# Performance work log

Measured on AMD Instinct MI355X. Metric: run time of the kernel, lower is better.

The kernel has to match this reference:

```python
import jax, jax.numpy as jnp
import numpy as np

K = 3  # kernel_size
S = 1  # stride
P = 1  # padding


def setup_inputs() -> dict:
    key = jax.random.key(0)
    ks = jax.random.split(key, 5)
    B, C, H, W, O = 4, 64, 128, 128, 64
    x = jax.random.normal(ks[0], (B, C, H, W), jnp.float32)
    # offset conv params (module inits these to 0; use small random values so the
    # bilinear-gather path is actually exercised with non-integer offsets)
    w_off = jax.random.normal(ks[1], (2 * K * K, C, K, K), jnp.float32) * 0.01
    b_off = jax.random.normal(ks[2], (2 * K * K,), jnp.float32) * 0.01
    # deformable conv params (torchvision DeformConv2d has bias=True by default)
    w_dcn = jax.random.normal(ks[3], (O, C, K, K), jnp.float32) * (1.0 / np.sqrt(C * K * K))
    b_dcn = jax.random.normal(ks[4], (O,), jnp.float32) * 0.01
    return {"x": x, "w_off": w_off, "b_off": b_off, "w_dcn": w_dcn, "b_dcn": b_dcn}


def _conv(x, w, b):
    y = jax.lax.conv_general_dilated(
        x, w, window_strides=(S, S), padding=[(P, P), (P, P)],
        dimension_numbers=("NCHW", "OIHW", "NCHW"))
    return y + b[None, :, None, None]


def _deform_conv2d(x, offset, w_dcn, b_dcn):
    # x: [B,C,H,W]; offset: [B, 2*K*K, Ho, Wo] with (dy, dx) interleaved per
    # kernel tap (row-major kh*K+kw), matching torchvision deform_conv2d.
    B, C, H, W = x.shape
    Ho, Wo = offset.shape[2], offset.shape[3]
    K2 = K * K
    off = offset.reshape(B, K2, 2, Ho, Wo)
    oy, ox = off[:, :, 0], off[:, :, 1]  # [B,K2,Ho,Wo]

    kh = (jnp.arange(K2) // K).astype(jnp.float32)
    kw = (jnp.arange(K2) % K).astype(jnp.float32)
    base_y = (jnp.arange(Ho) * S - P).astype(jnp.float32)
    base_x = (jnp.arange(Wo) * S - P).astype(jnp.float32)
    # fractional sampling locations: p0 + p_k + offset
    py = base_y[None, None, :, None] + kh[None, :, None, None] + oy  # [B,K2,Ho,Wo]
    px = base_x[None, None, None, :] + kw[None, :, None, None] + ox

    y0f = jnp.floor(py); x0f = jnp.floor(px)
    dy = py - y0f; dx = px - x0f
    y0 = y0f.astype(jnp.int32); x0 = x0f.astype(jnp.int32)

    def gather(yi, xi):
        # implicit zero padding: mask out-of-range corners
        valid = (yi >= 0) & (yi < H) & (xi >= 0) & (xi < W)
        yc = jnp.clip(yi, 0, H - 1)
        xc = jnp.clip(xi, 0, W - 1)
        v = jax.vmap(lambda xb, yb, xib: xb[:, yb, xib])(x, yc, xc)  # [B,C,K2,Ho,Wo]
        return v * valid[:, None].astype(x.dtype)

    v00 = gather(y0, x0)
    v01 = gather(y0, x0 + 1)
    v10 = gather(y0 + 1, x0)
    v11 = gather(y0 + 1, x0 + 1)

    wy = dy[:, None]; wx = dx[:, None]  # [B,1,K2,Ho,Wo]
    sampled = (v00 * (1 - wy) * (1 - wx) + v01 * (1 - wy) * wx
               + v10 * wy * (1 - wx) + v11 * wy * wx)  # [B,C,K2,Ho,Wo]

    O = w_dcn.shape[0]
    out = jnp.einsum("bckij,ock->boij", sampled, w_dcn.reshape(O, C, K2))
    return out + b_dcn[None, :, None, None]


def reference(x, w_off, b_off, w_dcn, b_dcn):
    offset = _conv(x, w_off, b_off)          # [B, 2*K*K, Ho, Wo]
    return _deform_conv2d(x, offset, w_dcn, b_dcn)
```

## Files before the change

kernel.cpp:

```cpp
#include <hip/hip_runtime.h>
#include <hip/hip_fp16.h>

#define B_ 4
#define H_ 128
#define W_ 128
#define HW_ 16384

typedef _Float16 half8 __attribute__((ext_vector_type(8)));
typedef float floatx16 __attribute__((ext_vector_type(16)));
typedef __attribute__((address_space(3))) void lds_void;
typedef const __attribute__((address_space(1))) void gbl_void;


__global__ __launch_bounds__(256) void k_prep(
    const float* __restrict__ x, const float* __restrict__ w_dcn,
    const float* __restrict__ w_off,
    __half* __restrict__ W2L, __half* __restrict__ W0L,
    _Float16* __restrict__ xh)
{
    int bid = blockIdx.x;
    int t = threadIdx.x;
    if (bid < 2048) {
        int idx = bid*256 + t;
        int p  = idx & (HW_-1);
        int bc = idx >> 14;
        const float* s = x + (size_t)bc*8*HW_ + p;
        half8 vv;
        #pragma unroll
        for (int e = 0; e < 8; ++e) vv[e] = (_Float16)s[e*HW_];
        *(half8*)(xh + (size_t)idx*8) = vv;
    } else {
        int idx = (bid - 2048)*256 + t;
        if (idx < 36864) {
            int e = idx & 7, lane = (idx>>3) & 63, og = (idx>>9) & 1;
            int ks = (idx>>10) & 3, tap = idx >> 12;
            int o = og*32 + (lane & 31);
            int c = ks*16 + (lane >> 5)*8 + e;
            W2L[idx] = __float2half(w_dcn[o*576 + c*9 + tap]);
        } else {
            int i2 = idx - 36864;
            int e = i2 & 7, lane = (i2>>3) & 63;
            int ks = (i2>>9) & 3, tap = i2 >> 11;
            int oc = lane & 31;
            int c = ks*16 + (lane >> 5)*8 + e;
            W0L[i2] = (oc < 18) ? __float2half(w_off[oc*576 + c*9 + tap])
                                : __float2half(0.f);
        }
    }
}

#define CHS2 3456
#define WLOC_OFF 27648
#define SMEM_SZ 36864

__global__ __launch_bounds__(128, 2) void k_fused(
    const float* __restrict__ x, const _Float16* __restrict__ xh,
    const _Float16* __restrict__ W2L, const _Float16* __restrict__ W0L,
    const float* __restrict__ b_off, const float* __restrict__ b_dcn,
    float* __restrict__ out)
{
    __shared__ __attribute__((aligned(16))) char smem[SMEM_SZ];
    char* halo_c = smem;

    int t = threadIdx.x;
    int lane = t & 63;
    int v = __builtin_amdgcn_readfirstlane(t >> 6);
    int c31 = lane & 31;
    int h8  = lane >> 5;

    char*  wl   = smem + WLOC_OFF + v*4608;
    float* offL = (float*)wl;
    char*  desc = wl;

    int bid  = blockIdx.x;
    int xcd  = bid & 7, sidx = bid >> 3;
    int orig = xcd*128 + sidx;
    int b    = orig >> 8;
    int rem  = orig & 255;
    int i0   = (rem >> 2) * 2;
    int j0   = (rem & 3) * 32;

    const float* xf = x + (size_t)b * (64*HW_);

    {
        int nst  = 14 - v;
        int base = v * 14;
        const _Float16* xhb = xh + ((size_t)b << 20);
        for (int s = 0; s < nst; ++s) {
            int i   = base + s;
            int idx = (i << 6) + lane;
            int ch  = idx / 216;
            int pl  = idx - ch*216;
            int hr  = pl / 36;
            int hx  = pl - hr*36;
            int grow = min(max(i0 - 2 + hr, 0), H_-1);
            int gcol = min(max(j0 - 2 + hx, 0), W_-1);
            const _Float16* g = xhb + ((size_t)ch << 17) + (size_t)(((grow<<7) + gcol) << 3);
            __builtin_amdgcn_global_load_lds((gbl_void*)g,
                                             (lds_void*)(halo_c + (i << 10)),
                                             16, 0, 0);
        }
    }
    __syncthreads();

    floatx16 accA = {0.f,0.f,0.f,0.f,0.f,0.f,0.f,0.f,0.f,0.f,0.f,0.f,0.f,0.f,0.f,0.f};
    const half8 hz = {0,0,0,0,0,0,0,0};
    #pragma unroll
    for (int tap = 0; tap < 9; ++tap) {
        int kh = tap/3, kw = tap - (tap/3)*3;
        int ii = i0 + v - 1 + kh;
        int jj = j0 + c31 - 1 + kw;
        bool valid = (ii >= 0) && (ii < H_) && (jj >= 0) && (jj < W_);
        int pixA = (v + 1 + kh)*36 + (c31 + 1 + kw);
        #pragma unroll
        for (int s = 0; s < 4; ++s) {
            half8 a = *(const half8*)(halo_c + (s*2 + h8)*CHS2 + pixA*16);
            a = valid ? a : hz;
            half8 bf = *(const half8*)(W0L + ((tap*4+s)<<9) + (lane<<3));
            accA = __builtin_amdgcn_mfma_f32_32x32x16_f16(a, bf, accA, 0, 0, 0);
        }
    }
    {
        int oc = c31;
        if (oc < 18) {
            float bo = b_off[oc];
            #pragma unroll
            for (int r = 0; r < 16; ++r) {
                int row = (r & 3) + 8*(r >> 2) + 4*h8;
                offL[row*18 + oc] = accA[r] + bo;
            }
        }
    }

    float2 o2r[5];
    #pragma unroll
    for (int e = 0; e < 5; ++e) {
        int idx = e*64 + lane;
        if (idx < 288) {
            int pl = idx / 9, tap = idx - pl*9;
            o2r[e] = *(const float2*)(offL + pl*18 + 2*tap);
        }
    }
    uint4 dreg[5];
    #pragma unroll
    for (int e = 0; e < 5; ++e) {
        int idx = e*64 + lane;
        if (idx < 288) {
            int pl = idx / 9, tap = idx - pl*9;
            int kh = tap/3, kw = tap - (tap/3)*3;
            float py = (float)(i0 + v - 1 + kh) + o2r[e].x;
            float px = (float)(j0 + pl - 1 + kw) + o2r[e].y;
            float y0f = floorf(py), x0f = floorf(px);
            float dy = py - y0f, dx = px - x0f;
            int y0 = (int)y0f, x0i = (int)x0f;
            int y1 = y0 + 1,  x1 = x0i + 1;
            bool vy0 = (y0>=0)&(y0<H_),   vy1 = (y1>=0)&(y1<H_);
            bool vx0 = (x0i>=0)&(x0i<W_), vx1 = (x1>=0)&(x1<W_);
            int yc0 = min(max(y0,0),H_-1),  yc1 = min(max(y1,0),H_-1);
            int xc0 = min(max(x0i,0),W_-1), xc1 = min(max(x1,0),W_-1);
            float w00 = (1.f-dy)*(1.f-dx) * ((vy0&&vx0)?1.f:0.f);
            float w01 = (1.f-dy)*dx       * ((vy0&&vx1)?1.f:0.f);
            float w10 = dy*(1.f-dx)       * ((vy1&&vx0)?1.f:0.f);
            float w11 = dy*dx             * ((vy1&&vx1)?1.f:0.f);
            int hy0 = yc0 - (i0-2), hy1 = yc1 - (i0-2);
            int hx0 = xc0 - (j0-2), hx1 = xc1 - (j0-2);
            bool inh = ((unsigned)hy0 < 6u) & ((unsigned)hy1 < 6u)
                     & ((unsigned)hx0 < 36u) & ((unsigned)hx1 < 36u);
            unsigned a0,a1,a2,a3;
            if (inh) { a0 = hy0*36+hx0; a1 = hy0*36+hx1; a2 = hy1*36+hx0; a3 = hy1*36+hx1; }
            else     { a0 = ((yc0<<7)+xc0) | 0x8000u; a1 = (yc0<<7)+xc1;
                       a2 = (yc1<<7)+xc0;             a3 = (yc1<<7)+xc1; }
            __half2 hw0 = __floats2half2_rn(w00, w01);
            __half2 hw1 = __floats2half2_rn(w10, w11);
            dreg[e].x = a0 | (a1 << 16);
            dreg[e].y = a2 | (a3 << 16);
            dreg[e].z = *(unsigned*)&hw0;
            dreg[e].w = *(unsigned*)&hw1;
        }
    }
    #pragma unroll
    for (int e = 0; e < 5; ++e) {
        int idx = e*64 + lane;
        if (idx < 288) {
            int pl = idx / 9, tap = idx - pl*9;
            *(uint4*)(desc + (tap*32 + pl)*16) = dreg[e];
        }
    }

    floatx16 acc0 = {0.f,0.f,0.f,0.f,0.f,0.f,0.f,0.f,0.f,0.f,0.f,0.f,0.f,0.f,0.f,0.f};
    floatx16 acc1 = acc0;

    const char* hqs0 = halo_c + (0*2 + h8)*CHS2;
    const char* hqs1 = halo_c + (1*2 + h8)*CHS2;
    const char* hqs2 = halo_c + (2*2 + h8)*CHS2;
    const char* hqs3 = halo_c + (3*2 + h8)*CHS2;

    #pragma unroll 3
    for (int tap = 0; tap < 9; ++tap) {
        uint4 d = *(const uint4*)(desc + (tap*32 + c31)*16);
        unsigned p0i = d.x & 0x7fffu, p1i = d.x >> 16;
        unsigned p2i = d.y & 0xffffu, p3i = d.y >> 16;
        bool inh = (d.x & 0x8000u) == 0u;
        unsigned short b00 = (unsigned short)(d.z & 0xffffu);
        unsigned short b01 = (unsigned short)(d.z >> 16);
        unsigned short b10 = (unsigned short)(d.w & 0xffffu);
        unsigned short b11 = (unsigned short)(d.w >> 16);
        _Float16 h00 = *(_Float16*)&b00, h01 = *(_Float16*)&b01;
        _Float16 h10 = *(_Float16*)&b10, h11 = *(_Float16*)&b11;
        half8 W00 = {h00,h00,h00,h00,h00,h00,h00,h00};
        half8 W01 = {h01,h01,h01,h01,h01,h01,h01,h01};
        half8 W10 = {h10,h10,h10,h10,h10,h10,h10,h10};
        half8 W11 = {h11,h11,h11,h11,h11,h11,h11,h11};
        half8 sk[4];
        const char* hb[4] = {hqs0, hqs1, hqs2, hqs3};
        #pragma unroll
        for (int s = 0; s < 4; ++s) {
            half8 v00, v01, v10, v11;
            if (inh) {
                v00 = *(const half8*)(hb[s] + p0i*16);
                v01 = *(const half8*)(hb[s] + p1i*16);
                v10 = *(const half8*)(hb[s] + p2i*16);
                v11 = *(const half8*)(hb[s] + p3i*16);
            } else {
                int chb = (s*2 + h8)*8;
                #pragma unroll
                for (int e = 0; e < 8; ++e) {
                    v00[e] = (_Float16)xf[(chb+e)*HW_ + (int)p0i];
                    v01[e] = (_Float16)xf[(chb+e)*HW_ + (int)p1i];
                    v10[e] = (_Float16)xf[(chb+e)*HW_ + (int)p2i];
                    v11[e] = (_Float16)xf[(chb+e)*HW_ + (int)p3i];
                }
            }
            sk[s] = v00*W00 + v01*W01 + v10*W10 + v11*W11;
        }
        #pragma unroll
        for (int s = 0; s < 4; ++s) {
            half8 bf0 = *(const half8*)(W2L + (((tap*4+s)*2+0)<<9) + (lane<<3));
            acc0 = __builtin_amdgcn_mfma_f32_32x32x16_f16(sk[s], bf0, acc0, 0, 0, 0);
            half8 bf1 = *(const half8*)(W2L + (((tap*4+s)*2+1)<<9) + (lane<<3));
            acc1 = __builtin_amdgcn_mfma_f32_32x32x16_f16(sk[s], bf1, acc1, 0, 0, 0);
        }
    }
    __syncthreads();

    float* E = (float*)smem;
    #pragma unroll
    for (int r = 0; r < 16; ++r) {
        int row = (r & 3) + 8*(r >> 2) + 4*h8;
        int pl  = v*32 + row;
        E[pl*66 + c31]      = acc0[r];
        E[pl*66 + 32 + c31] = acc1[r];
    }
    __syncthreads();
    int obase = (b*64)*HW_ + i0*W_ + j0;
    int prow = (lane >> 5)*W_ + c31;
    #pragma unroll
    for (int rep = 0; rep < 32; ++rep) {
        int o = rep*2 + v;
        out[obase + o*HW_ + prow] = E[lane*66 + o] + b_dcn[o];
    }
}

extern "C" void kernel_launch(void* const* d_in, const int* in_sizes, int n_in,
                              void* d_out, int out_size, void* d_ws, size_t ws_size,
                              hipStream_t stream) {
    const float* x     = (const float*)d_in[0];
    const float* w_off = (const float*)d_in[1];
    const float* b_off = (const float*)d_in[2];
    const float* w_dcn = (const float*)d_in[3];
    const float* b_dcn = (const float*)d_in[4];
    float* out = (float*)d_out;

    __half* W2L = (__half*)d_ws;
    __half* W0L = (__half*)((char*)d_ws + 73728);
    _Float16* xh = (_Float16*)((char*)d_ws + 110592);

    k_prep<<<2264, 256, 0, stream>>>(x, w_dcn, w_off, W2L, W0L, xh);
    k_fused<<<1024, 128, 0, stream>>>(x, xh, (const _Float16*)W2L,
                                      (const _Float16*)W0L, b_off, b_dcn, out);
}
```

Baseline: 92.04 us.

## Split channel reduction across four waves per block with LDS partial-sum combine

Doubles the block to 256 threads so each output row is handled by two waves that each reduce over half of the input channels, then combines the partial accumulators through shared memory. Only half the waves compute the offset conv and sampling descriptors, and the others wait at an added barrier. The out-of-halo fallback now reads packed fp16 channel-vector data instead of eight scalar fp32 loads. The aim is more waves in flight per CU to hide LDS and gather latency, at the cost of extra barriers, idle waves during the offset phase and an LDS reduction step.

```diff
diff --git a/kernel.cpp b/kernel.cpp
--- a/kernel.cpp
+++ b/kernel.cpp
@@ -53,7 +53,7 @@
 #define WLOC_OFF 27648
 #define SMEM_SZ 36864
 
-__global__ __launch_bounds__(128, 2) void k_fused(
+__global__ __launch_bounds__(256, 3) void k_fused(
     const float* __restrict__ x, const _Float16* __restrict__ xh,
     const _Float16* __restrict__ W2L, const _Float16* __restrict__ W0L,
     const float* __restrict__ b_off, const float* __restrict__ b_dcn,
@@ -64,11 +64,13 @@
 
     int t = threadIdx.x;
     int lane = t & 63;
-    int v = __builtin_amdgcn_readfirstlane(t >> 6);
+    int w = __builtin_amdgcn_readfirstlane(t >> 6);
+    int row   = w & 1;
+    int khalf = w >> 1;
     int c31 = lane & 31;
     int h8  = lane >> 5;
 
-    char*  wl   = smem + WLOC_OFF + v*4608;
+    char*  wl   = smem + WLOC_OFF + row*4608;
     float* offL = (float*)wl;
     char*  desc = wl;
 
@@ -80,14 +82,9 @@
     int i0   = (rem >> 2) * 2;
     int j0   = (rem & 3) * 32;
 
-    const float* xf = x + (size_t)b * (64*HW_);
-
     {
-        int nst  = 14 - v;
-        int base = v * 14;
         const _Float16* xhb = xh + ((size_t)b << 20);
-        for (int s = 0; s < nst; ++s) {
-            int i   = base + s;
+        for (int i = w; i < 27; i += 4) {
             int idx = (i << 6) + lane;
             int ch  = idx / 216;
             int pl  = idx - ch*216;
@@ -103,97 +100,100 @@
     }
     __syncthreads();
 
-    floatx16 accA = {0.f,0.f,0.f,0.f,0.f,0.f,0.f,0.f,0.f,0.f,0.f,0.f,0.f,0.f,0.f,0.f};
-    const half8 hz = {0,0,0,0,0,0,0,0};
-    #pragma unroll
-    for (int tap = 0; tap < 9; ++tap) {
-        int kh = tap/3, kw = tap - (tap/3)*3;
-        int ii = i0 + v - 1 + kh;
-        int jj = j0 + c31 - 1 + kw;
-        bool valid = (ii >= 0) && (ii < H_) && (jj >= 0) && (jj < W_);
-        int pixA = (v + 1 + kh)*36 + (c31 + 1 + kw);
-        #pragma unroll
-        for (int s = 0; s < 4; ++s) {
-            half8 a = *(const half8*)(halo_c + (s*2 + h8)*CHS2 + pixA*16);
-            a = valid ? a : hz;
-            half8 bf = *(const half8*)(W0L + ((tap*4+s)<<9) + (lane<<3));
-            accA = __builtin_amdgcn_mfma_f32_32x32x16_f16(a, bf, accA, 0, 0, 0);
-        }
-    }
-    {
-        int oc = c31;
-        if (oc < 18) {
-            float bo = b_off[oc];
+    if (khalf == 0) {
+        floatx16 accA = {0.f,0.f,0.f,0.f,0.f,0.f,0.f,0.f,0.f,0.f,0.f,0.f,0.f,0.f,0.f,0.f};
+        const half8 hz = {0,0,0,0,0,0,0,0};
+        #pragma unroll 3
+        for (int tap = 0; tap < 9; ++tap) {
+            int kh = tap/3, kw = tap - (tap/3)*3;
+            int ii = i0 + row - 1 + kh;
+            int jj = j0 + c31 - 1 + kw;
+            bool valid = (ii >= 0) && (ii < H_) && (jj >= 0) && (jj < W_);
+            int pixA = (row + 1 + kh)*36 + (c31 + 1 + kw);
             #pragma unroll
-            for (int r = 0; r < 16; ++r) {
-                int row = (r & 3) + 8*(r >> 2) + 4*h8;
-                offL[row*18 + oc] = accA[r] + bo;
-            }
-        }
-    }
-
-    float2 o2r[5];
-    #pragma unroll
-    for (int e = 0; e < 5; ++e) {
-        int idx = e*64 + lane;
-        if (idx < 288) {
-            int pl = idx / 9, tap = idx - pl*9;
-            o2r[e] = *(const float2*)(offL + pl*18 + 2*tap);
-        }
-    }
-    uint4 dreg[5];
-    #pragma unroll
-    for (int e = 0; e < 5; ++e) {
-        int idx = e*64 + lane;
-        if (idx < 288) {
-            int pl = idx / 9, tap = idx - pl*9;
-            int kh = tap/3, kw = tap - (tap/3)*3;
-            float py = (float)(i0 + v - 1 + kh) + o2r[e].x;
-            float px = (float)(j0 + pl - 1 + kw) + o2r[e].y;
-            float y0f = floorf(py), x0f = floorf(px);
-            float dy = py - y0f, dx = px - x0f;
-            int y0 = (int)y0f, x0i = (int)x0f;
-            int y1 = y0 + 1,  x1 = x0i + 1;
-            bool vy0 = (y0>=0)&(y0<H_),   vy1 = (y1>=0)&(y1<H_);
-            bool vx0 = (x0i>=0)&(x0i<W_), vx1 = (x1>=0)&(x1<W_);
-            int yc0 = min(max(y0,0),H_-1),  yc1 = min(max(y1,0),H_-1);
-            int xc0 = min(max(x0i,0),W_-1), xc1 = min(max(x1,0),W_-1);
-            float w00 = (1.f-dy)*(1.f-dx) * ((vy0&&vx0)?1.f:0.f);
-            float w01 = (1.f-dy)*dx       * ((vy0&&vx1)?1.f:0.f);
-            float w10 = dy*(1.f-dx)       * ((vy1&&vx0)?1.f:0.f);
-            float w11 = dy*dx             * ((vy1&&vx1)?1.f:0.f);
-            int hy0 = yc0 - (i0-2), hy1 = yc1 - (i0-2);
-            int hx0 = xc0 - (j0-2), hx1 = xc1 - (j0-2);
-            bool inh = ((unsigned)hy0 < 6u) & ((unsigned)hy1 < 6u)
-                     & ((unsigned)hx0 < 36u) & ((unsigned)hx1 < 36u);
-            unsigned a0,a1,a2,a3;
-            if (inh) { a0 = hy0*36+hx0; a1 = hy0*36+hx1; a2 = hy1*36+hx0; a3 = hy1*36+hx1; }
-            else     { a0 = ((yc0<<7)+xc0) | 0x8000u; a1 = (yc0<<7)+xc1;
-                       a2 = (yc1<<7)+xc0;             a3 = (yc1<<7)+xc1; }
-            __half2 hw0 = __floats2half2_rn(w00, w01);
-            __half2 hw1 = __floats2half2_rn(w10, w11);
-            dreg[e].x = a0 | (a1 << 16);
-            dreg[e].y = a2 | (a3 << 16);
-            dreg[e].z = *(unsigned*)&hw0;
-            dreg[e].w = *(unsigned*)&hw1;
-        }
-    }
-    #pragma unroll
-    for (int e = 0; e < 5; ++e) {
-        int idx = e*64 + lane;
-        if (idx < 288) {
-            int pl = idx / 9, tap = idx - pl*9;
-            *(uint4*)(desc + (tap*32 + pl)*16) = dreg[e];
-        }
-    }
+            for (int s = 0; s < 4; ++s) {
+                half8 a = *(const half8*)(halo_c + (s*2 + h8)*CHS2 + pixA*16);
+                a = valid ? a : hz;
+                half8 bf = *(const half8*)(W0L + ((tap*4+s)<<9) + (lane<<3));
+                accA = __builtin_amdgcn_mfma_f32_32x32x16_f16(a, bf, accA, 0, 0, 0);
+            }
+        }
+        {
+            int oc = c31;
+            if (oc < 18) {
+                float bo = b_off[oc];
+                #pragma unroll
+                for (int r = 0; r < 16; ++r) {
+                    int rr = (r & 3) + 8*(r >> 2) + 4*h8;
+                    offL[rr*18 + oc] = accA[r] + bo;
+                }
+            }
+        }
+        float2 o2r[5];
+        #pragma unroll
+        for (int e = 0; e < 5; ++e) {
+            int idx = e*64 + lane;
+            if (idx < 288) {
+                int pl = idx / 9, tap = idx - pl*9;
+                o2r[e] = *(const float2*)(offL + pl*18 + 2*tap);
+            }
+        }
+        uint4 dreg[5];
+        #pragma unroll
+        for (int e = 0; e < 5; ++e) {
+            int idx = e*64 + lane;
+            if (idx < 288) {
+                int pl = idx / 9, tap = idx - pl*9;
+                int kh = tap/3, kw = tap - (tap/3)*3;
+                float py = (float)(i0 + row - 1 + kh) + o2r[e].x;
+                float px = (float)(j0 + pl - 1 + kw) + o2r[e].y;
+                float y0f = floorf(py), x0f = floorf(px);
+                float dy = py - y0f, dx = px - x0f;
+                int y0 = (int)y0f, x0i = (int)x0f;
+                int y1 = y0 + 1,  x1 = x0i + 1;
+                bool vy0 = (y0>=0)&(y0<H_),   vy1 = (y1>=0)&(y1<H_);
+                bool vx0 = (x0i>=0)&(x0i<W_), vx1 = (x1>=0)&(x1<W_);
+                int yc0 = min(max(y0,0),H_-1),  yc1 = min(max(y1,0),H_-1);
+                int xc0 = min(max(x0i,0),W_-1), xc1 = min(max(x1,0),W_-1);
+                float w00 = (1.f-dy)*(1.f-dx) * ((vy0&&vx0)?1.f:0.f);
+                float w01 = (1.f-dy)*dx       * ((vy0&&vx1)?1.f:0.f);
+                float w10 = dy*(1.f-dx)       * ((vy1&&vx0)?1.f:0.f);
+                float w11 = dy*dx             * ((vy1&&vx1)?1.f:0.f);
+                int hy0 = yc0 - (i0-2), hy1 = yc1 - (i0-2);
+                int hx0 = xc0 - (j0-2), hx1 = xc1 - (j0-2);
+                bool inh = ((unsigned)hy0 < 6u) & ((unsigned)hy1 < 6u)
+                         & ((unsigned)hx0 < 36u) & ((unsigned)hx1 < 36u);
+                unsigned a0,a1,a2,a3;
+                if (inh) { a0 = hy0*36+hx0; a1 = hy0*36+hx1; a2 = hy1*36+hx0; a3 = hy1*36+hx1; }
+                else     { a0 = ((yc0<<7)+xc0) | 0x8000u; a1 = (yc0<<7)+xc1;
+                           a2 = (yc1<<7)+xc0;             a3 = (yc1<<7)+xc1; }
+                __half2 hw0 = __floats2half2_rn(w00, w01);
+                __half2 hw1 = __floats2half2_rn(w10, w11);
+                dreg[e].x = a0 | (a1 << 16);
+                dreg[e].y = a2 | (a3 << 16);
+                dreg[e].z = *(unsigned*)&hw0;
+                dreg[e].w = *(unsigned*)&hw1;
+            }
+        }
+        #pragma unroll
+        for (int e = 0; e < 5; ++e) {
+            int idx = e*64 + lane;
+            if (idx < 288) {
+                int pl = idx / 9, tap = idx - pl*9;
+                *(uint4*)(desc + (tap*32 + pl)*16) = dreg[e];
+            }
+        }
+    }
+    __syncthreads();
 
     floatx16 acc0 = {0.f,0.f,0.f,0.f,0.f,0.f,0.f,0.f,0.f,0.f,0.f,0.f,0.f,0.f,0.f,0.f};
     floatx16 acc1 = acc0;
 
-    const char* hqs0 = halo_c + (0*2 + h8)*CHS2;
-    const char* hqs1 = halo_c + (1*2 + h8)*CHS2;
-    const char* hqs2 = halo_c + (2*2 + h8)*CHS2;
-    const char* hqs3 = halo_c + (3*2 + h8)*CHS2;
+    int sA = khalf*2, sB = sA + 1;
+    const char* hq0 = halo_c + (sA*2 + h8)*CHS2;
+    const char* hq1 = halo_c + (sB*2 + h8)*CHS2;
+    const _Float16* xqA = xh + (((size_t)(b*8) + sA*2 + h8) << 17);
+    const _Float16* xqB = xh + (((size_t)(b*8) + sB*2 + h8) << 17);
 
     #pragma unroll 3
     for (int tap = 0; tap < 9; ++tap) {
@@ -211,52 +211,66 @@
         half8 W01 = {h01,h01,h01,h01,h01,h01,h01,h01};
         half8 W10 = {h10,h10,h10,h10,h10,h10,h10,h10};
         half8 W11 = {h11,h11,h11,h11,h11,h11,h11,h11};
-        half8 sk[4];
-        const char* hb[4] = {hqs0, hqs1, hqs2, hqs3};
-        #pragma unroll
-        for (int s = 0; s < 4; ++s) {
+        half8 sk[2];
+        const char* hb[2] = {hq0, hq1};
+        const _Float16* xq[2] = {xqA, xqB};
+        #pragma unroll
+        for (int s2 = 0; s2 < 2; ++s2) {
             half8 v00, v01, v10, v11;
             if (inh) {
-                v00 = *(const half8*)(hb[s] + p0i*16);
-                v01 = *(const half8*)(hb[s] + p1i*16);
-                v10 = *(const half8*)(hb[s] + p2i*16);
-                v11 = *(const half8*)(hb[s] + p3i*16);
+                v00 = *(const half8*)(hb[s2] + p0i*16);
+                v01 = *(const half8*)(hb[s2] + p1i*16);
+                v10 = *(const half8*)(hb[s2] + p2i*16);
+                v11 = *(const half8*)(hb[s2] + p3i*16);
             } else {
-                int chb = (s*2 + h8)*8;
-                #pragma unroll
-                for (int e = 0; e < 8; ++e) {
-                    v00[e] = (_Float16)xf[(chb+e)*HW_ + (int)p0i];
-                    v01[e] = (_Float16)xf[(chb+e)*HW_ + (int)p1i];
-                    v10[e] = (_Float16)xf[(chb+e)*HW_ + (int)p2i];
-                    v11[e] = (_Float16)xf[(chb+e)*HW_ + (int)p3i];
-                }
-            }
-            sk[s] = v00*W00 + v01*W01 + v10*W10 + v11*W11;
-        }
-        #pragma unroll
-        for (int s = 0; s < 4; ++s) {
+                v00 = *(const half8*)(xq[s2] + (size_t)p0i*8);
+                v01 = *(const half8*)(xq[s2] + (size_t)p1i*8);
+                v10 = *(const half8*)(xq[s2] + (size_t)p2i*8);
+                v11 = *(const half8*)(xq[s2] + (size_t)p3i*8);
+            }
+            sk[s2] = v00*W00 + v01*W01 + v10*W10 + v11*W11;
+        }
+        #pragma unroll
+        for (int s2 = 0; s2 < 2; ++s2) {
+            int s = sA + s2;
             half8 bf0 = *(const half8*)(W2L + (((tap*4+s)*2+0)<<9) + (lane<<3));
-            acc0 = __builtin_amdgcn_mfma_f32_32x32x16_f16(sk[s], bf0, acc0, 0, 0, 0);
+            acc0 = __builtin_amdgcn_mfma_f32_32x32x16_f16(sk[s2], bf0, acc0, 0, 0, 0);
             half8 bf1 = *(const half8*)(W2L + (((tap*4+s)*2+1)<<9) + (lane<<3));
-            acc1 = __builtin_amdgcn_mfma_f32_32x32x16_f16(sk[s], bf1, acc1, 0, 0, 0);
-        }
-    }
-    __syncthreads();
-
-    float* E = (float*)smem;
-    #pragma unroll
-    for (int r = 0; r < 16; ++r) {
-        int row = (r & 3) + 8*(r >> 2) + 4*h8;
-        int pl  = v*32 + row;
-        E[pl*66 + c31]      = acc0[r];
-        E[pl*66 + 32 + c31] = acc1[r];
-    }
-    __syncthreads();
+            acc1 = __builtin_amdgcn_mfma_f32_32x32x16_f16(sk[s2], bf1, acc1, 0, 0, 0);
+        }
+    }
+    __syncthreads();
+
+    float* P = (float*)smem;
+    if (khalf == 1) {
+        float* pr = P + row*2048;
+        #pragma unroll
+        for (int r = 0; r < 16; ++r) {
+            int pos = (r & 3) + 8*(r >> 2) + 4*h8;
+            pr[pos*64 + c31]      = acc0[r];
+            pr[pos*64 + 32 + c31] = acc1[r];
+        }
+    }
+    __syncthreads();
+
+    float* E = (float*)(smem + 16384);
+    if (khalf == 0) {
+        float* pr = P + row*2048;
+        #pragma unroll
+        for (int r = 0; r < 16; ++r) {
+            int pos = (r & 3) + 8*(r >> 2) + 4*h8;
+            int pl  = row*32 + pos;
+            E[pl*66 + c31]      = acc0[r] + pr[pos*64 + c31];
+            E[pl*66 + 32 + c31] = acc1[r] + pr[pos*64 + 32 + c31];
+        }
+    }
+    __syncthreads();
+
     int obase = (b*64)*HW_ + i0*W_ + j0;
     int prow = (lane >> 5)*W_ + c31;
     #pragma unroll
-    for (int rep = 0; rep < 32; ++rep) {
-        int o = rep*2 + v;
+    for (int rep = 0; rep < 16; ++rep) {
+        int o = rep*4 + w;
         out[obase + o*HW_ + prow] = E[lane*66 + o] + b_dcn[o];
     }
 }
@@ -276,6 +290,6 @@
     _Float16* xh = (_Float16*)((char*)d_ws + 110592);
 
     k_prep<<<2264, 256, 0, stream>>>(x, w_dcn, w_off, W2L, W0L, xh);
-    k_fused<<<1024, 128, 0, stream>>>(x, xh, (const _Float16*)W2L,
+    k_fused<<<1024, 256, 0, stream>>>(x, xh, (const _Float16*)W2L,
                                       (const _Float16*)W0L, b_off, b_dcn, out);
 }
```

Result: slower. 100.1 us (+8.8%).

## Drop LDS halo staging, gather directly from global fp16 with 16x16 MFMA tiles

Applied to the files above, without the earlier changes.

Removes the per-block LDS halo tile and its global_load_lds staging. Both the offset conv and the bilinear gathers now read channel-packed fp16 x straight from global memory (relying on cache), so the fp32 fallback path for out-of-halo samples is gone. Tiles become one row of 64 pixels with 4 waves of 16 pixels each, using 16x16x32 MFMAs with weights re-laid out to match. Block size doubles to 256 with a higher occupancy bound. The risk is more global and cache traffic per gather in exchange for less LDS use, better occupancy and no divergent fallback.

```diff
diff --git a/kernel.cpp b/kernel.cpp
--- a/kernel.cpp
+++ b/kernel.cpp
@@ -7,9 +7,7 @@
 #define HW_ 16384
 
 typedef _Float16 half8 __attribute__((ext_vector_type(8)));
-typedef float floatx16 __attribute__((ext_vector_type(16)));
-typedef __attribute__((address_space(3))) void lds_void;
-typedef const __attribute__((address_space(1))) void gbl_void;
+typedef float floatx4 __attribute__((ext_vector_type(4)));
 
 
 __global__ __launch_bounds__(256) void k_prep(
@@ -32,123 +30,115 @@
     } else {
         int idx = (bid - 2048)*256 + t;
         if (idx < 36864) {
-            int e = idx & 7, lane = (idx>>3) & 63, og = (idx>>9) & 1;
-            int ks = (idx>>10) & 3, tap = idx >> 12;
-            int o = og*32 + (lane & 31);
-            int c = ks*16 + (lane >> 5)*8 + e;
+            int e = idx & 7, lane = (idx>>3) & 63, og = (idx>>9) & 3;
+            int ks = (idx>>11) & 1, tap = idx >> 12;
+            int o = og*16 + (lane & 15);
+            int c = ks*32 + ((lane >> 4) & 3)*8 + e;
             W2L[idx] = __float2half(w_dcn[o*576 + c*9 + tap]);
         } else {
             int i2 = idx - 36864;
-            int e = i2 & 7, lane = (i2>>3) & 63;
-            int ks = (i2>>9) & 3, tap = i2 >> 11;
-            int oc = lane & 31;
-            int c = ks*16 + (lane >> 5)*8 + e;
+            int e = i2 & 7, lane = (i2>>3) & 63, og = (i2>>9) & 1;
+            int ks = (i2>>10) & 1, tap = i2 >> 11;
+            int oc = og*16 + (lane & 15);
+            int c = ks*32 + ((lane >> 4) & 3)*8 + e;
             W0L[i2] = (oc < 18) ? __float2half(w_off[oc*576 + c*9 + tap])
                                 : __float2half(0.f);
         }
     }
 }
 
-#define CHS2 3456
-#define WLOC_OFF 27648
-#define SMEM_SZ 36864
-
-__global__ __launch_bounds__(128, 2) void k_fused(
-    const float* __restrict__ x, const _Float16* __restrict__ xh,
+#define DESC_STRIDE 2304
+#define E_OFF 9216
+#define SMEM_SZ 26368
+
+__global__ __launch_bounds__(256, 4) void k_fused(
+    const _Float16* __restrict__ xh,
     const _Float16* __restrict__ W2L, const _Float16* __restrict__ W0L,
     const float* __restrict__ b_off, const float* __restrict__ b_dcn,
     float* __restrict__ out)
 {
     __shared__ __attribute__((aligned(16))) char smem[SMEM_SZ];
-    char* halo_c = smem;
 
     int t = threadIdx.x;
     int lane = t & 63;
-    int v = __builtin_amdgcn_readfirstlane(t >> 6);
-    int c31 = lane & 31;
-    int h8  = lane >> 5;
-
-    char*  wl   = smem + WLOC_OFF + v*4608;
-    float* offL = (float*)wl;
-    char*  desc = wl;
+    int w = __builtin_amdgcn_readfirstlane(t >> 6);
+    int c15 = lane & 15;
+    int q   = (lane >> 4) & 3;
+
+    char*  wreg = smem + w*DESC_STRIDE;
+    float* offL = (float*)wreg;
+    char*  desc = wreg;
 
     int bid  = blockIdx.x;
     int xcd  = bid & 7, sidx = bid >> 3;
     int orig = xcd*128 + sidx;
     int b    = orig >> 8;
     int rem  = orig & 255;
-    int i0   = (rem >> 2) * 2;
-    int j0   = (rem & 3) * 32;
-
-    const float* xf = x + (size_t)b * (64*HW_);
-
-    {
-        int nst  = 14 - v;
-        int base = v * 14;
-        const _Float16* xhb = xh + ((size_t)b << 20);
-        for (int s = 0; s < nst; ++s) {
-            int i   = base + s;
-            int idx = (i << 6) + lane;
-            int ch  = idx / 216;
-            int pl  = idx - ch*216;
-            int hr  = pl / 36;
-            int hx  = pl - hr*36;
-            int grow = min(max(i0 - 2 + hr, 0), H_-1);
-            int gcol = min(max(j0 - 2 + hx, 0), W_-1);
-            const _Float16* g = xhb + ((size_t)ch << 17) + (size_t)(((grow<<7) + gcol) << 3);
-            __builtin_amdgcn_global_load_lds((gbl_void*)g,
-                                             (lds_void*)(halo_c + (i << 10)),
-                                             16, 0, 0);
-        }
-    }
-    __syncthreads();
-
-    floatx16 accA = {0.f,0.f,0.f,0.f,0.f,0.f,0.f,0.f,0.f,0.f,0.f,0.f,0.f,0.f,0.f,0.f};
+    int i    = rem >> 1;
+    int j0b  = (rem & 1) * 64;
+    int j0   = j0b + w*16;
+
+    const _Float16* xq0 = xh + (((size_t)(b*8) + q    ) << 17);
+    const _Float16* xq1 = xh + (((size_t)(b*8) + 4 + q) << 17);
+
+    floatx4 accA0 = {0.f,0.f,0.f,0.f};
+    floatx4 accA1 = accA0;
     const half8 hz = {0,0,0,0,0,0,0,0};
-    #pragma unroll
+    #pragma unroll 3
     for (int tap = 0; tap < 9; ++tap) {
         int kh = tap/3, kw = tap - (tap/3)*3;
-        int ii = i0 + v - 1 + kh;
-        int jj = j0 + c31 - 1 + kw;
-        bool valid = (ii >= 0) && (ii < H_) && (jj >= 0) && (jj < W_);
-        int pixA = (v + 1 + kh)*36 + (c31 + 1 + kw);
-        #pragma unroll
-        for (int s = 0; s < 4; ++s) {
-            half8 a = *(const half8*)(halo_c + (s*2 + h8)*CHS2 + pixA*16);
+        int py = i - 1 + kh;
+        int px = j0 + c15 - 1 + kw;
+        bool valid = (py >= 0) && (py < H_) && (px >= 0) && (px < W_);
+        int pyc = min(max(py, 0), H_-1);
+        int pxc = min(max(px, 0), W_-1);
+        int pix = (pyc << 7) + pxc;
+        #pragma unroll
+        for (int ks = 0; ks < 2; ++ks) {
+            const _Float16* xq = ks ? xq1 : xq0;
+            half8 a = *(const half8*)(xq + (size_t)pix*8);
             a = valid ? a : hz;
-            half8 bf = *(const half8*)(W0L + ((tap*4+s)<<9) + (lane<<3));
-            accA = __builtin_amdgcn_mfma_f32_32x32x16_f16(a, bf, accA, 0, 0, 0);
+            half8 bf0 = *(const half8*)(W0L + ((tap*4 + ks*2 + 0)<<9) + (lane<<3));
+            half8 bf1 = *(const half8*)(W0L + ((tap*4 + ks*2 + 1)<<9) + (lane<<3));
+            accA0 = __builtin_amdgcn_mfma_f32_16x16x32_f16(a, bf0, accA0, 0, 0, 0);
+            accA1 = __builtin_amdgcn_mfma_f32_16x16x32_f16(a, bf1, accA1, 0, 0, 0);
         }
     }
     {
-        int oc = c31;
-        if (oc < 18) {
-            float bo = b_off[oc];
+        float bo0 = b_off[c15];
+        #pragma unroll
+        for (int r = 0; r < 4; ++r) {
+            int pos = q*4 + r;
+            offL[pos*18 + c15] = accA0[r] + bo0;
+        }
+        int oc1 = 16 + c15;
+        if (oc1 < 18) {
+            float bo1 = b_off[oc1];
             #pragma unroll
-            for (int r = 0; r < 16; ++r) {
-                int row = (r & 3) + 8*(r >> 2) + 4*h8;
-                offL[row*18 + oc] = accA[r] + bo;
+            for (int r = 0; r < 4; ++r) {
+                int pos = q*4 + r;
+                offL[pos*18 + oc1] = accA1[r] + bo1;
             }
         }
     }
 
-    float2 o2r[5];
-    #pragma unroll
-    for (int e = 0; e < 5; ++e) {
+    float2 o2r[3];
+    #pragma unroll
+    for (int e = 0; e < 3; ++e) {
         int idx = e*64 + lane;
-        if (idx < 288) {
+        if (idx < 144) {
             int pl = idx / 9, tap = idx - pl*9;
             o2r[e] = *(const float2*)(offL + pl*18 + 2*tap);
         }
     }
-    uint4 dreg[5];
-    #pragma unroll
-    for (int e = 0; e < 5; ++e) {
+    uint4 dreg[3];
+    #pragma unroll
+    for (int e = 0; e < 3; ++e) {
         int idx = e*64 + lane;
-        if (idx < 288) {
+        if (idx < 144) {
             int pl = idx / 9, tap = idx - pl*9;
             int kh = tap/3, kw = tap - (tap/3)*3;
-            float py = (float)(i0 + v - 1 + kh) + o2r[e].x;
+            float py = (float)(i - 1 + kh) + o2r[e].x;
             float px = (float)(j0 + pl - 1 + kw) + o2r[e].y;
             float y0f = floorf(py), x0f = floorf(px);
             float dy = py - y0f, dx = px - x0f;
@@ -162,14 +152,8 @@
             float w01 = (1.f-dy)*dx       * ((vy0&&vx1)?1.f:0.f);
             float w10 = dy*(1.f-dx)       * ((vy1&&vx0)?1.f:0.f);
             float w11 = dy*dx             * ((vy1&&vx1)?1.f:0.f);
-            int hy0 = yc0 - (i0-2), hy1 = yc1 - (i0-2);
-            int hx0 = xc0 - (j0-2), hx1 = xc1 - (j0-2);
-            bool inh = ((unsigned)hy0 < 6u) & ((unsigned)hy1 < 6u)
-                     & ((unsigned)hx0 < 36u) & ((unsigned)hx1 < 36u);
-            unsigned a0,a1,a2,a3;
-            if (inh) { a0 = hy0*36+hx0; a1 = hy0*36+hx1; a2 = hy1*36+hx0; a3 = hy1*36+hx1; }
-            else     { a0 = ((yc0<<7)+xc0) | 0x8000u; a1 = (yc0<<7)+xc1;
-                       a2 = (yc1<<7)+xc0;             a3 = (yc1<<7)+xc1; }
+            unsigned a0 = (yc0<<7)+xc0, a1 = (yc0<<7)+xc1;
+            unsigned a2 = (yc1<<7)+xc0, a3 = (yc1<<7)+xc1;
             __half2 hw0 = __floats2half2_rn(w00, w01);
             __half2 hw1 = __floats2half2_rn(w10, w11);
             dreg[e].x = a0 | (a1 << 16);
@@ -179,28 +163,22 @@
         }
     }
     #pragma unroll
-    for (int e = 0; e < 5; ++e) {
+    for (int e = 0; e < 3; ++e) {
         int idx = e*64 + lane;
-        if (idx < 288) {
+        if (idx < 144) {
             int pl = idx / 9, tap = idx - pl*9;
-            *(uint4*)(desc + (tap*32 + pl)*16) = dreg[e];
-        }
-    }
-
-    floatx16 acc0 = {0.f,0.f,0.f,0.f,0.f,0.f,0.f,0.f,0.f,0.f,0.f,0.f,0.f,0.f,0.f,0.f};
-    floatx16 acc1 = acc0;
-
-    const char* hqs0 = halo_c + (0*2 + h8)*CHS2;
-    const char* hqs1 = halo_c + (1*2 + h8)*CHS2;
-    const char* hqs2 = halo_c + (2*2 + h8)*CHS2;
-    const char* hqs3 = halo_c + (3*2 + h8)*CHS2;
+            *(uint4*)(desc + (pl*9 + tap)*16) = dreg[e];
+        }
+    }
+
+    floatx4 acc0 = {0.f,0.f,0.f,0.f};
+    floatx4 acc1 = acc0, acc2 = acc0, acc3 = acc0;
 
     #pragma unroll 3
     for (int tap = 0; tap < 9; ++tap) {
-        uint4 d = *(const uint4*)(desc + (tap*32 + c31)*16);
-        unsigned p0i = d.x & 0x7fffu, p1i = d.x >> 16;
-        unsigned p2i = d.y & 0xffffu, p3i = d.y >> 16;
-        bool inh = (d.x & 0x8000u) == 0u;
+        uint4 d = *(const uint4*)(desc + (c15*9 + tap)*16);
+        unsigned p0 = d.x & 0xffffu, p1 = d.x >> 16;
+        unsigned p2 = d.y & 0xffffu, p3 = d.y >> 16;
         unsigned short b00 = (unsigned short)(d.z & 0xffffu);
         unsigned short b01 = (unsigned short)(d.z >> 16);
         unsigned short b10 = (unsigned short)(d.w & 0xffffu);
@@ -211,53 +189,40 @@
         half8 W01 = {h01,h01,h01,h01,h01,h01,h01,h01};
         half8 W10 = {h10,h10,h10,h10,h10,h10,h10,h10};
         half8 W11 = {h11,h11,h11,h11,h11,h11,h11,h11};
-        half8 sk[4];
-        const char* hb[4] = {hqs0, hqs1, hqs2, hqs3};
-        #pragma unroll
-        for (int s = 0; s < 4; ++s) {
-            half8 v00, v01, v10, v11;
-            if (inh) {
-                v00 = *(const half8*)(hb[s] + p0i*16);
-                v01 = *(const half8*)(hb[s] + p1i*16);
-                v10 = *(const half8*)(hb[s] + p2i*16);
-                v11 = *(const half8*)(hb[s] + p3i*16);
-            } else {
-                int chb = (s*2 + h8)*8;
-                #pragma unroll
-                for (int e = 0; e < 8; ++e) {
-                    v00[e] = (_Float16)xf[(chb+e)*HW_ + (int)p0i];
-                    v01[e] = (_Float16)xf[(chb+e)*HW_ + (int)p1i];
-                    v10[e] = (_Float16)xf[(chb+e)*HW_ + (int)p2i];
-                    v11[e] = (_Float16)xf[(chb+e)*HW_ + (int)p3i];
-                }
-            }
-            sk[s] = v00*W00 + v01*W01 + v10*W10 + v11*W11;
-        }
-        #pragma unroll
-        for (int s = 0; s < 4; ++s) {
-            half8 bf0 = *(const half8*)(W2L + (((tap*4+s)*2+0)<<9) + (lane<<3));
-            acc0 = __builtin_amdgcn_mfma_f32_32x32x16_f16(sk[s], bf0, acc0, 0, 0, 0);
-            half8 bf1 = *(const half8*)(W2L + (((tap*4+s)*2+1)<<9) + (lane<<3));
-            acc1 = __builtin_amdgcn_mfma_f32_32x32x16_f16(sk[s], bf1, acc1, 0, 0, 0);
-        }
+        #pragma unroll
+        for (int s = 0; s < 2; ++s) {
+            const _Float16* xq = s ? xq1 : xq0;
+            half8 v00 = *(const half8*)(xq + (size_t)p0*8);
+            half8 v01 = *(const half8*)(xq + (size_t)p1*8);
+            half8 v10 = *(const half8*)(xq + (size_t)p2*8);
+            half8 v11 = *(const half8*)(xq + (size_t)p3*8);
+            half8 sk = v00*W00 + v01*W01 + v10*W10 + v11*W11;
+            half8 bfa = *(const half8*)(W2L + ((tap*8 + s*4 + 0)<<9) + (lane<<3));
+            acc0 = __builtin_amdgcn_mfma_f32_16x16x32_f16(sk, bfa, acc0, 0, 0, 0);
+            half8 bfb = *(const half8*)(W2L + ((tap*8 + s*4 + 1)<<9) + (lane<<3));
+            acc1 = __builtin_amdgcn_mfma_f32_16x16x32_f16(sk, bfb, acc1, 0, 0, 0);
+            half8 bfc = *(const half8*)(W2L + ((tap*8 + s*4 + 2)<<9) + (lane<<3));
+            acc2 = __builtin_amdgcn_mfma_f32_16x16x32_f16(sk, bfc, acc2, 0, 0, 0);
+            half8 bfd = *(const half8*)(W2L + ((tap*8 + s*4 + 3)<<9) + (lane<<3));
+            acc3 = __builtin_amdgcn_mfma_f32_16x16x32_f16(sk, bfd, acc3, 0, 0, 0);
+        }
+    }
+
+    float* E = (float*)(smem + E_OFF);
+    #pragma unroll
+    for (int r = 0; r < 4; ++r) {
+        int pl = w*16 + q*4 + r;
+        E[pl*67 + c15]      = acc0[r];
+        E[pl*67 + 16 + c15] = acc1[r];
+        E[pl*67 + 32 + c15] = acc2[r];
+        E[pl*67 + 48 + c15] = acc3[r];
     }
     __syncthreads();
-
-    float* E = (float*)smem;
-    #pragma unroll
-    for (int r = 0; r < 16; ++r) {
-        int row = (r & 3) + 8*(r >> 2) + 4*h8;
-        int pl  = v*32 + row;
-        E[pl*66 + c31]      = acc0[r];
-        E[pl*66 + 32 + c31] = acc1[r];
-    }
-    __syncthreads();
-    int obase = (b*64)*HW_ + i0*W_ + j0;
-    int prow = (lane >> 5)*W_ + c31;
-    #pragma unroll
-    for (int rep = 0; rep < 32; ++rep) {
-        int o = rep*2 + v;
-        out[obase + o*HW_ + prow] = E[lane*66 + o] + b_dcn[o];
+    int obase = (b*64)*HW_ + i*W_ + j0b;
+    #pragma unroll
+    for (int rep = 0; rep < 16; ++rep) {
+        int o = rep*4 + w;
+        out[obase + o*HW_ + lane] = E[lane*67 + o] + b_dcn[o];
     }
 }
 
@@ -276,6 +241,6 @@
     _Float16* xh = (_Float16*)((char*)d_ws + 110592);
 
     k_prep<<<2264, 256, 0, stream>>>(x, w_dcn, w_off, W2L, W0L, xh);
-    k_fused<<<1024, 128, 0, stream>>>(x, xh, (const _Float16*)W2L,
+    k_fused<<<1024, 256, 0, stream>>>((const _Float16*)xh, (const _Float16*)W2L,
                                       (const _Float16*)W0L, b_off, b_dcn, out);
 }
```

Result: slower. 109.6 us (+19.1%).
